# Optimization experiments

Measured on AMD Instinct MI355X. Metric: run time of the kernel, lower is better.

Reference implementation:

```python
import jax, jax.numpy as jnp
import numpy as np

EPS = 1e-5


def _conv3d(x, w, b):
    # torch Conv3d(padding='same'): total pad k-1, left = (k-1)//2 (0 for k=2), rest on right
    k = w.shape[-1]
    lo = (k - 1) // 2
    hi = (k - 1) - lo
    y = jax.lax.conv_general_dilated(
        x, w, window_strides=(1, 1, 1), padding=[(lo, hi)] * 3,
        dimension_numbers=('NCDHW', 'OIDHW', 'NCDHW'))
    return y + b[None, :, None, None, None]


def _cksn(x, w, b):
    # Conv3d -> InstanceNorm3d (no affine, biased var) -> ReLU
    y = _conv3d(x, w, b)
    m = y.mean(axis=(2, 3, 4), keepdims=True)
    v = y.var(axis=(2, 3, 4), keepdims=True)
    return jax.nn.relu((y - m) * jax.lax.rsqrt(v + EPS))


def _pixel_shuffle3d(x, s):
    b, c, d, h, w = x.shape
    n = c // s ** 3
    x = x.reshape(b, n, s, s, s, d, h, w)
    x = x.transpose(0, 1, 5, 2, 6, 3, 7, 4)
    return x.reshape(b, n, d * s, h * s, w * s)


def _box_filter(x, n):
    # grouped conv3d with ones kernel, padding='same' (odd n -> symmetric), / n^3
    s = jax.lax.reduce_window(x, 0.0, jax.lax.add,
                              (1, 1, n, n, n), (1, 1, 1, 1, 1), 'SAME')
    return s / float(n ** 3)


def reference(x, q1_w, q1_b, q2_w, q2_b, k1_w, k1_b, k2_w, k2_b, v_w, v_b):
    U = 2    # upscale
    N = 3    # neighbor
    K3 = 8   # kernelsize^3
    b, c, h, d, w = x.shape

    # q branch: two cksn blocks -> (b, (2*U)^3, h, d, w) -> pixelshuffle -> (b, 8, 2h, 2d, 2w)
    q = _cksn(_cksn(x, q1_w, q1_b), q2_w, q2_b)
    q = _pixel_shuffle3d(q, U)

    # k branch: -> (b, U^3, h, d, w) -> pixelshuffle -> (b, 1, 2h, 2d, 2w)
    k = _cksn(_cksn(x, k1_w, k1_b), k2_w, k2_b)
    k = _pixel_shuffle3d(k, U)

    # matmul over (8,1)x(1,1) == broadcast product over the single k channel
    qk = _box_filter(q * k, N)                       # (b, 8, 2h, 2d, 2w)

    # v branch: conv to c*8 channels then nearest-neighbor x2 upsample
    v = _cksn(x, v_w, v_b)                           # (b, c*8, h, d, w)
    v = jnp.repeat(jnp.repeat(jnp.repeat(v, 2, axis=2), 2, axis=3), 2, axis=4)
    v = v.reshape(b, c, K3, 2 * h, 2 * d, 2 * w)     # channel split (c, 8)

    # matmul (c,8)@(8,1): contract the 8 shuffle positions
    qkv = jnp.einsum('bcjhdw,bjhdw->bchdw', v, qk)   # (b, c, 2h, 2d, 2w)
    return _box_filter(qkv, N)


def setup_inputs() -> dict:
    key = jax.random.key(0)
    C, K = 64, 2
    ks = jax.random.split(key, 12)

    def w(k, o, i):
        return jax.random.normal(k, (o, i, K, K, K), dtype=jnp.float32) * 0.05

    def bias(k, o):
        return jax.random.normal(k, (o,), dtype=jnp.float32) * 0.05

    return {
        'x': jax.random.normal(ks[0], (1, C, 32, 32, 32), dtype=jnp.float32),
        'q1_w': w(ks[1], C // 4, C), 'q1_b': bias(ks[2], C // 4),
        'q2_w': w(ks[3], 64, C // 4), 'q2_b': bias(ks[4], 64),   # (2*upscale)^3 = 64
        'k1_w': w(ks[5], C // 4, C), 'k1_b': bias(ks[6], C // 4),
        'k2_w': w(ks[7], 8, C // 4), 'k2_b': bias(ks[8], 8),     # upscale^3 = 8
        'v_w': w(ks[9], C * 8, C), 'v_b': bias(ks[10], C * 8),
    }
```

## Files before the change

### kernel.cpp

```cpp
#include <hip/hip_runtime.h>
#include <hip/hip_bf16.h>


constexpr int VOX = 32 * 32 * 32;
constexpr float INV_VOX = 1.0f / 32768.0f;
constexpr float EPSF = 1e-5f;

typedef __attribute__((ext_vector_type(8))) short s16x8;
typedef __attribute__((ext_vector_type(4))) float f32x4;

static __device__ __forceinline__ ushort bf16_bits(float v) {
  __hip_bfloat16 h = __float2bfloat16(v);
  return *reinterpret_cast<ushort*>(&h);
}

__global__ __launch_bounds__(256) void prep_all_kernel(
    const float* __restrict__ x,
    const float* __restrict__ vw,
    const float* __restrict__ q1w, const float* __restrict__ q1b,
    const float* __restrict__ k1w, const float* __restrict__ k1b,
    const float* __restrict__ q2w, const float* __restrict__ q2b,
    const float* __restrict__ k2w, const float* __restrict__ k2b,
    ushort* __restrict__ xh, ushort* __restrict__ xl,
    ushort* __restrict__ wfh, ushort* __restrict__ wfl,
    ushort* __restrict__ wqh, ushort* __restrict__ wql, float* __restrict__ bqk,
    ushort* __restrict__ w2h, ushort* __restrict__ w2l, float* __restrict__ b96)
{
  __shared__ float ts[64][65];
  const int t = threadIdx.x;
  if ((int)blockIdx.x < 512) {
    const int vox0 = blockIdx.x * 64;
#pragma unroll
    for (int i = 0; i < 16; ++i) {
      int e = i * 256 + t;
      int ci = e >> 6, vl = e & 63;
      ts[ci][vl] = x[(size_t)ci * VOX + vox0 + vl];
    }
    __syncthreads();
    const int vl = t >> 2, cig = t & 3;
    uint h[8], l[8];
#pragma unroll
    for (int p = 0; p < 8; ++p) {
      float v0 = ts[cig * 16 + 2 * p][vl];
      float v1 = ts[cig * 16 + 2 * p + 1][vl];
      ushort h0 = bf16_bits(v0), h1 = bf16_bits(v1);
      float r0 = v0 - __bfloat162float(*reinterpret_cast<__hip_bfloat16*>(&h0));
      float r1 = v1 - __bfloat162float(*reinterpret_cast<__hip_bfloat16*>(&h1));
      h[p] = (uint)h0 | ((uint)h1 << 16);
      l[p] = (uint)bf16_bits(r0) | ((uint)bf16_bits(r1) << 16);
    }
    size_t base = (size_t)(vox0 + vl) * 64 + cig * 16;
    *reinterpret_cast<uint4*>(xh + base)     = make_uint4(h[0], h[1], h[2], h[3]);
    *reinterpret_cast<uint4*>(xh + base + 8) = make_uint4(h[4], h[5], h[6], h[7]);
    *reinterpret_cast<uint4*>(xl + base)     = make_uint4(l[0], l[1], l[2], l[3]);
    *reinterpret_cast<uint4*>(xl + base + 8) = make_uint4(l[4], l[5], l[6], l[7]);
    return;
  }
  const int bid = blockIdx.x - 512;
  if (bid < 128) {
    int tid = bid * 256 + t;
    int oc = tid & 511, g = (tid >> 9) & 3, khalf = (tid >> 11) & 1, tap = tid >> 12;
    uint h[4], l[4];
#pragma unroll
    for (int p = 0; p < 4; ++p) {
      int ci0 = khalf * 32 + g * 8 + 2 * p;
      float v0 = vw[oc * 512 + ci0 * 8 + tap];
      float v1 = vw[oc * 512 + (ci0 + 1) * 8 + tap];
      ushort h0 = bf16_bits(v0), h1 = bf16_bits(v1);
      float r0 = v0 - __bfloat162float(*reinterpret_cast<__hip_bfloat16*>(&h0));
      float r1 = v1 - __bfloat162float(*reinterpret_cast<__hip_bfloat16*>(&h1));
      h[p] = (uint)h0 | ((uint)h1 << 16);
      l[p] = (uint)bf16_bits(r0) | ((uint)bf16_bits(r1) << 16);
    }
    size_t base = (size_t)tid * 8;
    *reinterpret_cast<uint4*>(wfh + base) = make_uint4(h[0], h[1], h[2], h[3]);
    *reinterpret_cast<uint4*>(wfl + base) = make_uint4(l[0], l[1], l[2], l[3]);
  } else if (bid < 136) {
    int tid = (bid - 128) * 256 + t;
    if (tid < 32) bqk[tid] = tid < 16 ? q1b[tid] : k1b[tid - 16];
    int oc = tid & 31, g = (tid >> 5) & 3, khalf = (tid >> 7) & 1, tap = tid >> 8;
    const float* src = oc < 16 ? q1w + oc * 512 : k1w + (oc - 16) * 512;
    uint h[4], l[4];
#pragma unroll
    for (int p = 0; p < 4; ++p) {
      int ci0 = khalf * 32 + g * 8 + 2 * p;
      float v0 = src[ci0 * 8 + tap];
      float v1 = src[(ci0 + 1) * 8 + tap];
      ushort h0 = bf16_bits(v0), h1 = bf16_bits(v1);
      float r0 = v0 - __bfloat162float(*reinterpret_cast<__hip_bfloat16*>(&h0));
      float r1 = v1 - __bfloat162float(*reinterpret_cast<__hip_bfloat16*>(&h1));
      h[p] = (uint)h0 | ((uint)h1 << 16);
      l[p] = (uint)bf16_bits(r0) | ((uint)bf16_bits(r1) << 16);
    }
    size_t base = (size_t)tid * 8;
    *reinterpret_cast<uint4*>(wqh + base) = make_uint4(h[0], h[1], h[2], h[3]);
    *reinterpret_cast<uint4*>(wql + base) = make_uint4(l[0], l[1], l[2], l[3]);
  } else {
    int tid = (bid - 136) * 256 + t;
    if (tid < 96) b96[tid] = tid < 64 ? q2b[tid] : (tid < 72 ? k2b[tid - 64] : 0.f);
    int oc = tid % 96, g = (tid / 96) & 3, kslot = tid / 384;
    int khalf = kslot & 1, tap = kslot >> 1;
    uint h[4], l[4];
#pragma unroll
    for (int p = 0; p < 4; ++p) {
      float v[2];
#pragma unroll
      for (int q = 0; q < 2; ++q) {
        int ci = khalf * 32 + g * 8 + 2 * p + q;
        float w = 0.f;
        if (ci < 16) { if (oc < 64) w = q2w[(oc * 16 + ci) * 8 + tap]; }
        else if (ci < 32) {
          if (oc >= 64 && oc < 72) w = k2w[((oc - 64) * 16 + (ci - 16)) * 8 + tap];
        }
        v[q] = w;
      }
      ushort h0 = bf16_bits(v[0]), h1 = bf16_bits(v[1]);
      float r0 = v[0] - __bfloat162float(*reinterpret_cast<__hip_bfloat16*>(&h0));
      float r1 = v[1] - __bfloat162float(*reinterpret_cast<__hip_bfloat16*>(&h1));
      h[p] = (uint)h0 | ((uint)h1 << 16);
      l[p] = (uint)bf16_bits(r0) | ((uint)bf16_bits(r1) << 16);
    }
    size_t base = (size_t)tid * 8;
    *reinterpret_cast<uint4*>(w2h + base) = make_uint4(h[0], h[1], h[2], h[3]);
    *reinterpret_cast<uint4*>(w2l + base) = make_uint4(l[0], l[1], l[2], l[3]);
  }
}

__global__ __launch_bounds__(256) void xprep2_kernel(
    const float* __restrict__ qk1, const float* __restrict__ np,
    ushort* __restrict__ xh, ushort* __restrict__ xl)
{
  __shared__ float ts[32][65];
  const int t = threadIdx.x;
  const int vox0 = blockIdx.x * 64;
#pragma unroll
  for (int i = 0; i < 8; ++i) {
    int e = i * 256 + t;
    int ci = e >> 6, vl = e & 63;
    float m = np[2 * ci], rs = np[2 * ci + 1];
    float v = qk1[(size_t)ci * VOX + vox0 + vl];
    ts[ci][vl] = fmaxf((v - m) * rs, 0.f);
  }
  __syncthreads();
  const int vl = t >> 2, cig = t & 3;
  uint h[8], l[8];
#pragma unroll
  for (int p = 0; p < 8; ++p) {
    if (cig < 2) {
      float v0 = ts[cig * 16 + 2 * p][vl];
      float v1 = ts[cig * 16 + 2 * p + 1][vl];
      ushort h0 = bf16_bits(v0), h1 = bf16_bits(v1);
      float r0 = v0 - __bfloat162float(*reinterpret_cast<__hip_bfloat16*>(&h0));
      float r1 = v1 - __bfloat162float(*reinterpret_cast<__hip_bfloat16*>(&h1));
      h[p] = (uint)h0 | ((uint)h1 << 16);
      l[p] = (uint)bf16_bits(r0) | ((uint)bf16_bits(r1) << 16);
    } else { h[p] = 0u; l[p] = 0u; }
  }
  size_t base = (size_t)(vox0 + vl) * 64 + cig * 16;
  *reinterpret_cast<uint4*>(xh + base)     = make_uint4(h[0], h[1], h[2], h[3]);
  *reinterpret_cast<uint4*>(xh + base + 8) = make_uint4(h[4], h[5], h[6], h[7]);
  *reinterpret_cast<uint4*>(xl + base)     = make_uint4(l[0], l[1], l[2], l[3]);
  *reinterpret_cast<uint4*>(xl + base + 8) = make_uint4(l[4], l[5], l[6], l[7]);
}

template <int NMF, int OCS>
__device__ __forceinline__ void conv_mfma_body(
    ushort* Bs,
    const ushort* __restrict__ xh, const ushort* __restrict__ xl,
    const ushort* __restrict__ wh, const ushort* __restrict__ wl,
    const float* __restrict__ bias, float* __restrict__ y,
    float* __restrict__ part, int bx, int nt, int t)
{
  const int wave = t >> 6, lane = t & 63;
  const int wm = wave >> 1, wn = wave & 1;
  const int g = lane >> 4, ww = lane & 15;
  const int m0 = bx * (NMF * 32);
  const int td = nt >> 4, th = (nt >> 1) & 7, tw = nt & 1;
  const int d0 = td * 2, h0 = th * 4, w0 = tw * 16;

  for (int i = 0; i < 16; ++i) {
    int c = i * 256 + t;
    if (c < 4080) {
      int split = (c >= 2040) ? 1 : 0;
      int c2 = c - split * 2040;
      int pos = c2 >> 3, cig = c2 & 7;
      int dz = pos / 85, rem = pos - dz * 85;
      int hz = rem / 17, wz = rem - hz * 17;
      int d = d0 + dz, h = h0 + hz, w = w0 + wz;
      uint4 val = make_uint4(0, 0, 0, 0);
      if (d < 32 && h < 32 && w < 32) {
        const ushort* src = split ? xl : xh;
        val = *reinterpret_cast<const uint4*>(
            src + (size_t)(d * 1024 + h * 32 + w) * 64 + cig * 8);
      }
      int addr = (pos << 7) + cig * 16;
      addr ^= (pos & 7) << 4;
      *reinterpret_cast<uint4*>(
          reinterpret_cast<char*>(Bs) + split * 32640 + addr) = val;
    }
  }
  __syncthreads();

  const int ocl = m0 + wm * (NMF * 16) + ww;
  f32x4 acc[NMF][4];
#pragma unroll
  for (int mf = 0; mf < NMF; ++mf)
#pragma unroll
    for (int hh = 0; hh < 4; ++hh) acc[mf][hh] = (f32x4){0.f, 0.f, 0.f, 0.f};

  for (int tap = 0; tap < 8; ++tap) {
    const int kd = tap >> 2, kh = (tap >> 1) & 1, kw = tap & 1;
#pragma unroll
    for (int khalf = 0; khalf < 2; ++khalf) {
      const size_t abase = ((size_t)((tap * 2 + khalf) * 4 + g) * OCS + ocl) * 8;
      s16x8 Ah[NMF], Al[NMF];
#pragma unroll
      for (int mf = 0; mf < NMF; ++mf) {
        Ah[mf] = *reinterpret_cast<const s16x8*>(wh + abase + mf * 16 * 8);
        Al[mf] = *reinterpret_cast<const s16x8*>(wl + abase + mf * 16 * 8);
      }
      const int srow = ((wn + kd) * 5 + kh) * 17 + kw;
#pragma unroll
      for (int hh = 0; hh < 4; ++hh) {
        int pos = srow + hh * 17 + ww;
        int baddr = (pos << 7) + khalf * 64 + g * 16;
        baddr ^= (pos & 7) << 4;
        const char* bp = reinterpret_cast<const char*>(Bs) + baddr;
        s16x8 Bh = *reinterpret_cast<const s16x8*>(bp);
        s16x8 Bl = *reinterpret_cast<const s16x8*>(bp + 32640);
#pragma unroll
        for (int mf = 0; mf < NMF; ++mf) {
          acc[mf][hh] = __builtin_amdgcn_mfma_f32_16x16x32_bf16(
              Ah[mf], Bh, acc[mf][hh], 0, 0, 0);
          acc[mf][hh] = __builtin_amdgcn_mfma_f32_16x16x32_bf16(
              Al[mf], Bh, acc[mf][hh], 0, 0, 0);
          acc[mf][hh] = __builtin_amdgcn_mfma_f32_16x16x32_bf16(
              Ah[mf], Bl, acc[mf][hh], 0, 0, 0);
        }
      }
    }
  }

  float bs[NMF][4];
#pragma unroll
  for (int mf = 0; mf < NMF; ++mf)
#pragma unroll
    for (int reg = 0; reg < 4; ++reg)
      bs[mf][reg] = bias[m0 + wm * (NMF * 16) + mf * 16 + g * 4 + reg];

  float ssum[NMF][4], ssq[NMF][4];
#pragma unroll
  for (int mf = 0; mf < NMF; ++mf)
#pragma unroll
    for (int reg = 0; reg < 4; ++reg) { ssum[mf][reg] = 0.f; ssq[mf][reg] = 0.f; }

#pragma unroll
  for (int mf = 0; mf < NMF; ++mf) {
#pragma unroll
    for (int hh = 0; hh < 4; ++hh) {
      int vox = (d0 + wn) * 1024 + (h0 + hh) * 32 + w0 + ww;
#pragma unroll
      for (int reg = 0; reg < 4; ++reg) {
        float v = acc[mf][hh][reg] + bs[mf][reg];
        int oc = m0 + wm * (NMF * 16) + mf * 16 + g * 4 + reg;
        y[(size_t)oc * VOX + vox] = v;
        ssum[mf][reg] += v;
        ssq[mf][reg] += v * v;
      }
    }
  }
#pragma unroll
  for (int mf = 0; mf < NMF; ++mf)
#pragma unroll
    for (int reg = 0; reg < 4; ++reg)
#pragma unroll
      for (int off = 1; off < 16; off <<= 1) {
        ssum[mf][reg] += __shfl_xor(ssum[mf][reg], off);
        ssq[mf][reg]  += __shfl_xor(ssq[mf][reg], off);
      }
  if ((lane & 15) == 0) {
    float* pp = part + (size_t)(nt * 2 + wn) * (OCS * 2);
#pragma unroll
    for (int mf = 0; mf < NMF; ++mf)
#pragma unroll
      for (int reg = 0; reg < 4; ++reg) {
        int oc = m0 + wm * (NMF * 16) + mf * 16 + g * 4 + reg;
        pp[oc * 2]     = ssum[mf][reg];
        pp[oc * 2 + 1] = ssq[mf][reg];
      }
  }
}

__global__ __launch_bounds__(256) void conv_fused_kernel(
    const ushort* __restrict__ xh, const ushort* __restrict__ xl,
    const ushort* __restrict__ wfh, const ushort* __restrict__ wfl,
    const float* __restrict__ vb, float* __restrict__ vraw,
    float* __restrict__ part_v,
    const ushort* __restrict__ wqh, const ushort* __restrict__ wql,
    const float* __restrict__ bqk, float* __restrict__ qk1,
    float* __restrict__ part_qk)
{
  __shared__ ushort Bs[2 * 255 * 64];
  const int bx = blockIdx.x, nt = blockIdx.y, t = threadIdx.x;
  if (bx < 2)
    conv_mfma_body<8, 512>(Bs, xh, xl, wfh, wfl, vb, vraw, part_v, bx, nt, t);
  else
    conv_mfma_body<1, 32>(Bs, xh, xl, wqh, wql, bqk, qk1, part_qk, 0, nt, t);
}

template <int NMF, int OCS>
__global__ __launch_bounds__(256) void conv_v_mfma(
    const ushort* __restrict__ xh, const ushort* __restrict__ xl,
    const ushort* __restrict__ wh, const ushort* __restrict__ wl,
    const float* __restrict__ bias, float* __restrict__ y,
    float* __restrict__ part)
{
  __shared__ ushort Bs[2 * 255 * 64];
  conv_mfma_body<NMF, OCS>(Bs, xh, xl, wh, wl, bias, y, part,
                           blockIdx.x, blockIdx.y, threadIdx.x);
}

__global__ __launch_bounds__(256) void finalize3_kernel(
    const float* __restrict__ p1, int C1, int NT1, float* __restrict__ n1,
    const float* __restrict__ p2, int C2, int NT2, float* __restrict__ n2,
    const float* __restrict__ p3, int C3, int NT3, float* __restrict__ n3)
{
  const int t = threadIdx.x;
  const int chl = t >> 4, w = t & 15;
  const int g = blockIdx.x * 16 + chl;

  const float* part = nullptr; float* np = nullptr; int C = 0, NT = 0, c = 0;
  if (g < C1)                { part = p1; np = n1; C = C1; NT = NT1; c = g; }
  else if (g < C1 + C2)      { part = p2; np = n2; C = C2; NT = NT2; c = g - C1; }
  else if (g < C1 + C2 + C3) { part = p3; np = n3; C = C3; NT = NT3; c = g - C1 - C2; }

  float s = 0.f, ss = 0.f;
  if (part)
    for (int tile = w; tile < NT; tile += 16) {
      float2 v = *reinterpret_cast<const float2*>(&part[((size_t)tile * C + c) * 2]);
      s += v.x; ss += v.y;
    }
#pragma unroll
  for (int off = 1; off < 16; off <<= 1) {
    s  += __shfl_xor(s, off);
    ss += __shfl_xor(ss, off);
  }
  if (w == 0 && part) {
    float m = s * INV_VOX;
    float var = ss * INV_VOX - m * m;
    np[2 * c]     = m;
    np[2 * c + 1] = rsqrtf(var + EPSF);
  }
}

__global__ __launch_bounds__(256) void qk_box_kernel(
    const float* __restrict__ qraw, const float* __restrict__ npq,
    const float* __restrict__ kraw, const float* __restrict__ npk,
    float* __restrict__ qkout)
{
  __shared__ float s[1000];
  __shared__ float ws2[800];
  const int j = blockIdx.y;
  const int tile = blockIdx.x;
  const int W0 = (tile & 7) * 8, H0 = ((tile >> 3) & 7) * 8, D0 = (tile >> 6) * 8;
  const int t = threadIdx.x;
  const int cbD = (D0 >> 1) - 1, cbH = (H0 >> 1) - 1, cbW = (W0 >> 1) - 1;
  const float2* npq2 = reinterpret_cast<const float2*>(npq);
  const float2* npk2 = reinterpret_cast<const float2*>(npk);

#pragma unroll
  for (int kk = 0; kk < 7; ++kk) {
    int f = t + kk * 256;
    if (f < 1728) {
      int par = f / 216, idx = f - par * 216;
      int dz = idx / 36, r2 = idx - dz * 36, hz = r2 / 6, wz = r2 - hz * 6;
      int pd = (par >> 2) & 1, ph = (par >> 1) & 1, pw = par & 1;
      int dzf = 2 * dz + pd - 1, hzf = 2 * hz + ph - 1, wzf = 2 * wz + pw - 1;
      if ((unsigned)dzf < 10u && (unsigned)hzf < 10u && (unsigned)wzf < 10u) {
        int cD = cbD + dz, cH = cbH + hz, cW = cbW + wz;
        float prod = 0.f;
        if ((unsigned)cD < 32u && (unsigned)cH < 32u && (unsigned)cW < 32u) {
          int cidx = cD * 1024 + cH * 32 + cW;
          int qc = j * 8 + par;
          float2 nq = npq2[qc];
          float2 nk = npk2[par];
          float qv = fmaxf((qraw[(size_t)qc * VOX + cidx] - nq.x) * nq.y, 0.f);
          float kv = fmaxf((kraw[(size_t)par * VOX + cidx] - nk.x) * nk.y, 0.f);
          prod = qv * kv;
        }
        s[dzf * 100 + hzf * 10 + wzf] = prod;
      }
    }
  }
  __syncthreads();
#pragma unroll
  for (int i = 0; i < 4; ++i) {
    int e = t + i * 256;
    if (e < 800) {
      int dz = e / 80, r2 = e - dz * 80, hz = r2 >> 3, wz1 = r2 & 7;
      int base = dz * 100 + hz * 10 + wz1;
      ws2[e] = s[base] + s[base + 1] + s[base + 2];
    }
  }
  __syncthreads();
#pragma unroll
  for (int rep = 0; rep < 2; ++rep) {
    int o = t + rep * 256;
    int wz = o & 7, hz = (o >> 3) & 7, dz = o >> 6;
    int wb = dz * 80 + hz * 8 + wz;
    float sum = 0.f;
#pragma unroll
    for (int a = 0; a < 3; ++a)
      sum += ws2[wb + a * 80] + ws2[wb + a * 80 + 8] + ws2[wb + a * 80 + 16];
    qkout[(size_t)j * 262144 + (D0 + dz) * 4096 + (H0 + hz) * 64 + (W0 + wz)] =
        sum * (1.f / 27.f);
  }
}

__global__ __launch_bounds__(256) void einsum_box_kernel(
    const float* __restrict__ vraw, const float* __restrict__ npv,
    const float* __restrict__ qk, float* __restrict__ out)
{
  __shared__ char vs_raw[2][6912];
  __shared__ float qkvs[1000];
  __shared__ float wsum[800];

  const int c0 = (blockIdx.x & 1) * 32;
  const int ciBase = ((blockIdx.x >> 1) & 1) * 16;
  const int tile = blockIdx.y;
  const int W0 = (tile & 7) * 8, H0 = ((tile >> 3) & 7) * 8, D0 = (tile >> 6) * 8;
  const int t = threadIdx.x;
  const int cbD = (D0 >> 1) - 1, cbH = (H0 >> 1) - 1, cbW = (W0 >> 1) - 1;
  const float2* npv2 = reinterpret_cast<const float2*>(npv);

  uint soff[7]; int sbyte[7]; int snidx[7]; bool svalid[7];
#pragma unroll
  for (int k = 0; k < 7; ++k) {
    int f = t + k * 256;
    int j = f / 216, idx = f - j * 216;
    int dz = idx / 36, r2 = idx - dz * 36, hz = r2 / 6, wz = r2 - hz * 6;
    int cD = cbD + dz, cH = cbH + hz, cW = cbW + wz;
    bool vld = (f < 1728) && (unsigned)cD < 32u && (unsigned)cH < 32u &&
               (unsigned)cW < 32u;
    svalid[k] = vld;
    soff[k] = vld ? (uint)((c0 * 8 + j) * VOX + cD * 1024 + cH * 32 + cW) : 0u;
    snidx[k] = (f < 1728) ? (c0 * 8 + j) : 0;
    int byte = idx * 32 + (j >> 2) * 16 + (j & 3) * 4;
    sbyte[k] = byte ^ (((idx >> 2) & 7) << 4);
  }

  int vbyte[4]; float qr[4][8];
#pragma unroll
  for (int i = 0; i < 4; ++i) {
    int pos = t + i * 256;
    vbyte[i] = 0;
#pragma unroll
    for (int j = 0; j < 8; ++j) qr[i][j] = 0.f;
    if (pos < 1000) {
      int dz = pos / 100, rem = pos - dz * 100, hz = rem / 10, wz = rem - hz * 10;
      int D = D0 - 1 + dz, H = H0 - 1 + hz, W = W0 - 1 + wz;
      if ((unsigned)D < 64u && (unsigned)H < 64u && (unsigned)W < 64u) {
        int fidx = D * 4096 + H * 64 + W;
#pragma unroll
        for (int j = 0; j < 8; ++j)
          qr[i][j] = qk[(size_t)j * 262144 + fidx];
        int vidx = ((D >> 1) - cbD) * 36 + ((H >> 1) - cbH) * 6 + ((W >> 1) - cbW);
        vbyte[i] = (vidx * 32) ^ (((vidx >> 2) & 7) << 4);
      }
    }
  }

  int wb[4];
#pragma unroll
  for (int i = 0; i < 4; ++i) {
    int e = t + i * 256;
    int dz = e / 80, r2 = e - dz * 80, hz = r2 >> 3, wz1 = r2 & 7;
    wb[i] = dz * 100 + hz * 10 + wz1;
  }
  int wb2[2]; float* op[2];
#pragma unroll
  for (int rep = 0; rep < 2; ++rep) {
    int o = t + rep * 256;
    int wz = o & 7, hz = (o >> 3) & 7, dz = o >> 6;
    wb2[rep] = dz * 80 + hz * 8 + wz;
    op[rep] = out + (size_t)c0 * 262144 +
              (D0 + dz) * 4096 + (H0 + hz) * 64 + (W0 + wz);
  }

  float pre[7];
  auto fetchv = [&](int ci) {
    const uint cio = (uint)(ci * 8 * VOX);
    const int cin8 = ci * 8;
#pragma unroll
    for (int k = 0; k < 7; ++k) {
      if (k < 6 || t < 192) {
        float2 mr = npv2[snidx[k] + cin8];
        float raw = vraw[soff[k] + cio];
        pre[k] = svalid[k] ? fmaxf((raw - mr.x) * mr.y, 0.f) : 0.f;
      }
    }
  };

  fetchv(ciBase);
#pragma unroll
  for (int k = 0; k < 7; ++k)
    if (k < 6 || t < 192)
      *reinterpret_cast<float*>(vs_raw[0] + sbyte[k]) = pre[k];
  fetchv(ciBase + 1);
  __syncthreads();

  for (int li = 0; li < 16; ++li) {
    const int ci = ciBase + li;
    const int cbuf = li & 1;
    if (li < 15) {
#pragma unroll
      for (int k = 0; k < 7; ++k)
        if (k < 6 || t < 192)
          *reinterpret_cast<float*>(vs_raw[cbuf ^ 1] + sbyte[k]) = pre[k];
      if (li < 14) fetchv(ci + 2);
    }
#pragma unroll
    for (int i = 0; i < 4; ++i) {
      int pos = t + i * 256;
      if (pos < 1000) {
        const char* vb0 = vs_raw[cbuf];
        float4 va = *reinterpret_cast<const float4*>(vb0 + vbyte[i]);
        float4 vb = *reinterpret_cast<const float4*>(vb0 + (vbyte[i] ^ 16));
        float val = qr[i][0] * va.x;
        val = fmaf(qr[i][1], va.y, val);
        val = fmaf(qr[i][2], va.z, val);
        val = fmaf(qr[i][3], va.w, val);
        val = fmaf(qr[i][4], vb.x, val);
        val = fmaf(qr[i][5], vb.y, val);
        val = fmaf(qr[i][6], vb.z, val);
        val = fmaf(qr[i][7], vb.w, val);
        qkvs[pos] = val;
      }
    }
    __syncthreads();
#pragma unroll
    for (int i = 0; i < 4; ++i) {
      if (i < 3 || t < 32) {
        int b = wb[i];
        wsum[t + i * 256] = qkvs[b] + qkvs[b + 1] + qkvs[b + 2];
      }
    }
    __syncthreads();
#pragma unroll
    for (int rep = 0; rep < 2; ++rep) {
      float sum = 0.f;
#pragma unroll
      for (int a = 0; a < 3; ++a)
        sum += wsum[wb2[rep] + a * 80] + wsum[wb2[rep] + a * 80 + 8] +
               wsum[wb2[rep] + a * 80 + 16];
      op[rep][(size_t)ci << 18] = sum * (1.f / 27.f);
    }
  }
}

extern "C" void kernel_launch(void* const* d_in, const int* in_sizes, int n_in,
                              void* d_out, int out_size, void* d_ws, size_t ws_size,
                              hipStream_t stream)
{
  (void)in_sizes; (void)n_in; (void)out_size; (void)ws_size;
  const float* x   = (const float*)d_in[0];
  const float* q1w = (const float*)d_in[1];
  const float* q1b = (const float*)d_in[2];
  const float* q2w = (const float*)d_in[3];
  const float* q2b = (const float*)d_in[4];
  const float* k1w = (const float*)d_in[5];
  const float* k1b = (const float*)d_in[6];
  const float* k2w = (const float*)d_in[7];
  const float* k2b = (const float*)d_in[8];
  const float* vw  = (const float*)d_in[9];
  const float* vb  = (const float*)d_in[10];
  float* out = (float*)d_out;

  float* p = (float*)d_ws;
  float* vraw    = p; p += (size_t)512 * VOX;
  float* regionR = p; p += (size_t)96 * VOX;
  float* qkbuf   = p; p += (size_t)8 * 262144;
  float* part_v  = p; p += (size_t)512 * 512 * 2;
  float* part_qk = p; p += (size_t)512 * 32 * 2;
  float* part96  = p; p += (size_t)512 * 96 * 2;
  float* WfF     = p; p += (size_t)262144;
  float* WqF     = p; p += (size_t)16384;
  float* W2F     = p; p += (size_t)49152;
  float* np_qk1  = p; p += 64;
  float* np96    = p; p += 192;
  float* np_v    = p; p += 1024;
  float* bqk     = p; p += 32;
  float* b96     = p; p += 96;

  float* qk1raw = regionR;
  float* y96    = regionR;

  ushort* xT_hi = (ushort*)qkbuf;
  ushort* xT_lo = (ushort*)qkbuf + (size_t)32768 * 64;
  ushort* Wf_hi = (ushort*)WfF;
  ushort* Wf_lo = (ushort*)WfF + 262144;
  ushort* Wq_hi = (ushort*)WqF;
  ushort* Wq_lo = (ushort*)WqF + 16384;
  ushort* W2_hi = (ushort*)W2F;
  ushort* W2_lo = (ushort*)W2F + 49152;

  dim3 blk(256);
  prep_all_kernel<<<672, blk, 0, stream>>>(
      x, vw, q1w, q1b, k1w, k1b, q2w, q2b, k2w, k2b,
      xT_hi, xT_lo, Wf_hi, Wf_lo, Wq_hi, Wq_lo, bqk, W2_hi, W2_lo, b96);
  conv_fused_kernel<<<dim3(3, 256), blk, 0, stream>>>(
      xT_hi, xT_lo, Wf_hi, Wf_lo, vb, vraw, part_v,
      Wq_hi, Wq_lo, bqk, qk1raw, part_qk);
  finalize3_kernel<<<34, blk, 0, stream>>>(
      part_v, 512, 512, np_v,
      part_qk, 32, 512, np_qk1,
      nullptr, 0, 0, nullptr);
  xprep2_kernel<<<512, blk, 0, stream>>>(qk1raw, np_qk1, xT_hi, xT_lo);
  conv_v_mfma<3, 96><<<dim3(1, 256), blk, 0, stream>>>(
      xT_hi, xT_lo, W2_hi, W2_lo, b96, y96, part96);
  finalize3_kernel<<<6, blk, 0, stream>>>(
      part96, 96, 512, np96,
      nullptr, 0, 0, nullptr,
      nullptr, 0, 0, nullptr);
  qk_box_kernel<<<dim3(512, 8), blk, 0, stream>>>(
      y96, np96, y96 + (size_t)64 * VOX, np96 + 128, qkbuf);
  einsum_box_kernel<<<dim3(4, 512), blk, 0, stream>>>(
      vraw, np_v, qkbuf, out);
}
```

Baseline: 278.5 us.

## Read v directly from global in einsum kernel, dropping LDS double buffer

Removes the double-buffered shared-memory staging of normalized v tiles along with its register prefetch. Each output position now reads its 8 raw v values from global memory (relying on cache) and applies the instance-norm/ReLU inline. This cuts LDS usage and the swizzled staging logic, but gives up the overlap of the next channel's loads with compute and adds redundant global loads, since neighboring positions share v voxels. A trailing barrier is added to protect qkvs reuse across iterations.

```diff
diff --git a/kernel.cpp b/kernel.cpp
--- a/kernel.cpp
+++ b/kernel.cpp
@@ -421,7 +421,6 @@
     const float* __restrict__ vraw, const float* __restrict__ npv,
     const float* __restrict__ qk, float* __restrict__ out)
 {
-  __shared__ char vs_raw[2][6912];
   __shared__ float qkvs[1000];
   __shared__ float wsum[800];
 
@@ -430,30 +429,13 @@
   const int tile = blockIdx.y;
   const int W0 = (tile & 7) * 8, H0 = ((tile >> 3) & 7) * 8, D0 = (tile >> 6) * 8;
   const int t = threadIdx.x;
-  const int cbD = (D0 >> 1) - 1, cbH = (H0 >> 1) - 1, cbW = (W0 >> 1) - 1;
   const float2* npv2 = reinterpret_cast<const float2*>(npv);
 
-  uint soff[7]; int sbyte[7]; int snidx[7]; bool svalid[7];
-#pragma unroll
-  for (int k = 0; k < 7; ++k) {
-    int f = t + k * 256;
-    int j = f / 216, idx = f - j * 216;
-    int dz = idx / 36, r2 = idx - dz * 36, hz = r2 / 6, wz = r2 - hz * 6;
-    int cD = cbD + dz, cH = cbH + hz, cW = cbW + wz;
-    bool vld = (f < 1728) && (unsigned)cD < 32u && (unsigned)cH < 32u &&
-               (unsigned)cW < 32u;
-    svalid[k] = vld;
-    soff[k] = vld ? (uint)((c0 * 8 + j) * VOX + cD * 1024 + cH * 32 + cW) : 0u;
-    snidx[k] = (f < 1728) ? (c0 * 8 + j) : 0;
-    int byte = idx * 32 + (j >> 2) * 16 + (j & 3) * 4;
-    sbyte[k] = byte ^ (((idx >> 2) & 7) << 4);
-  }
-
-  int vbyte[4]; float qr[4][8];
+  uint voff[4]; float qr[4][8];
 #pragma unroll
   for (int i = 0; i < 4; ++i) {
     int pos = t + i * 256;
-    vbyte[i] = 0;
+    voff[i] = 0u;
 #pragma unroll
     for (int j = 0; j < 8; ++j) qr[i][j] = 0.f;
     if (pos < 1000) {
@@ -464,8 +446,7 @@
 #pragma unroll
         for (int j = 0; j < 8; ++j)
           qr[i][j] = qk[(size_t)j * 262144 + fidx];
-        int vidx = ((D >> 1) - cbD) * 36 + ((H >> 1) - cbH) * 6 + ((W >> 1) - cbW);
-        vbyte[i] = (vidx * 32) ^ (((vidx >> 2) & 7) << 4);
+        voff[i] = (uint)((D >> 1) * 1024 + (H >> 1) * 32 + (W >> 1));
       }
     }
   }
@@ -487,53 +468,27 @@
               (D0 + dz) * 4096 + (H0 + hz) * 64 + (W0 + wz);
   }
 
-  float pre[7];
-  auto fetchv = [&](int ci) {
-    const uint cio = (uint)(ci * 8 * VOX);
-    const int cin8 = ci * 8;
-#pragma unroll
-    for (int k = 0; k < 7; ++k) {
-      if (k < 6 || t < 192) {
-        float2 mr = npv2[snidx[k] + cin8];
-        float raw = vraw[soff[k] + cio];
-        pre[k] = svalid[k] ? fmaxf((raw - mr.x) * mr.y, 0.f) : 0.f;
-      }
-    }
-  };
-
-  fetchv(ciBase);
-#pragma unroll
-  for (int k = 0; k < 7; ++k)
-    if (k < 6 || t < 192)
-      *reinterpret_cast<float*>(vs_raw[0] + sbyte[k]) = pre[k];
-  fetchv(ciBase + 1);
-  __syncthreads();
-
   for (int li = 0; li < 16; ++li) {
     const int ci = ciBase + li;
-    const int cbuf = li & 1;
-    if (li < 15) {
-#pragma unroll
-      for (int k = 0; k < 7; ++k)
-        if (k < 6 || t < 192)
-          *reinterpret_cast<float*>(vs_raw[cbuf ^ 1] + sbyte[k]) = pre[k];
-      if (li < 14) fetchv(ci + 2);
+    const size_t cbase = (size_t)(c0 + ci) * 8 * VOX;
+    float mj[8], rj[8];
+#pragma unroll
+    for (int j = 0; j < 8; ++j) {
+      float2 nv = npv2[(c0 + ci) * 8 + j];
+      mj[j] = nv.x; rj[j] = nv.y;
     }
 #pragma unroll
     for (int i = 0; i < 4; ++i) {
       int pos = t + i * 256;
       if (pos < 1000) {
-        const char* vb0 = vs_raw[cbuf];
-        float4 va = *reinterpret_cast<const float4*>(vb0 + vbyte[i]);
-        float4 vb = *reinterpret_cast<const float4*>(vb0 + (vbyte[i] ^ 16));
-        float val = qr[i][0] * va.x;
-        val = fmaf(qr[i][1], va.y, val);
-        val = fmaf(qr[i][2], va.z, val);
-        val = fmaf(qr[i][3], va.w, val);
-        val = fmaf(qr[i][4], vb.x, val);
-        val = fmaf(qr[i][5], vb.y, val);
-        val = fmaf(qr[i][6], vb.z, val);
-        val = fmaf(qr[i][7], vb.w, val);
+        const float* vp = vraw + cbase + voff[i];
+        float val = 0.f;
+#pragma unroll
+        for (int j = 0; j < 8; ++j) {
+          float raw = vp[(size_t)j * VOX];
+          float vn = fmaxf((raw - mj[j]) * rj[j], 0.f);
+          val = fmaf(qr[i][j], vn, val);
+        }
         qkvs[pos] = val;
       }
     }
@@ -555,6 +510,7 @@
                wsum[wb2[rep] + a * 80 + 16];
       op[rep][(size_t)ci << 18] = sum * (1.f / 27.f);
     }
+    __syncthreads();
   }
 }
 
```

Result: slower. 375.5 us (+34.9%).
